# Kernel optimization log

Hardware: AMD Instinct MI355X
Metric: run time of the kernel (lower is better)

## Reference

```python
import jax, jax.numpy as jnp
import numpy as np

LEN_MASK = 2   # hardcoded in the original forward
TOP_POOL = 5   # positions drawn from top-5 intensity slots


def setup_inputs() -> dict:
    key = jax.random.key(0)
    k1, k2 = jax.random.split(key)
    B, S = 16384, 1024
    x = jax.random.randint(k1, (B, S), 0, 10000, dtype=jnp.int64)
    intensity_ = jax.random.uniform(k2, (B, 1, S), dtype=jnp.float32)
    return {"x": x, "intensity_": intensity_, "max_pred": 5}


def reference(x, intensity_, max_pred):
    # x: [B, S] int token ids; intensity_: [B, 1, S] float
    intensity = jnp.squeeze(intensity_, axis=1)            # [B, S]
    B, S = x.shape
    # top-5 positions by descending intensity (== argsort(desc)[:5])
    top5 = jax.lax.top_k(intensity, TOP_POOL)[1]           # [B, 5] int
    # randperm(5)[:2] per sample, vectorized: argsort of iid uniforms
    rkey = jax.random.key(42)
    u = jax.random.uniform(rkey, (B, TOP_POOL))
    sel = jnp.argsort(u, axis=-1)[:, :LEN_MASK]            # [B, 2] random 2-of-5
    mask_pos2 = jnp.take_along_axis(top5, sel, axis=1)     # [B, 2]
    # mask_bool: all False (rand > 1), True at the chosen positions
    mask_bool = jnp.zeros((B, S), dtype=bool).at[
        jnp.arange(B)[:, None], mask_pos2
    ].set(True)                                            # [B, S]
    mask_x = jnp.where(mask_bool, jnp.asarray(1, x.dtype), x)   # masked_fill(x, mask_bool, 1)
    mask_token2 = jnp.take_along_axis(x, mask_pos2, axis=1)     # [B, 2]
    # pad to max_pred with zeros (original branch: len_mask < max_pred)
    n_pad = max_pred - LEN_MASK
    mask_pos = jnp.pad(mask_pos2, ((0, 0), (0, n_pad))).astype(jnp.int64)
    mask_token = jnp.pad(mask_token2, ((0, 0), (0, n_pad))).astype(jnp.int64)
    return mask_x, mask_token, mask_pos
```

## Files before the change

kernel.cpp:

```cpp
#include <hip/hip_runtime.h>
#include <stdint.h>


#define S_LEN 1024
#define TOPK 5

__device__ __forceinline__ uint32_t rotl32(uint32_t x, int r) {
    return (x << r) | (x >> (32 - r));
}

__device__ __forceinline__ void threefry2x32(uint32_t k0, uint32_t k1,
                                             uint32_t x0, uint32_t x1,
                                             uint32_t& o0, uint32_t& o1) {
    uint32_t ks2 = k0 ^ k1 ^ 0x1BD11BDAu;
    x0 += k0; x1 += k1;
#define TF_R4(a,b,c,d) \
    x0 += x1; x1 = rotl32(x1,a); x1 ^= x0; \
    x0 += x1; x1 = rotl32(x1,b); x1 ^= x0; \
    x0 += x1; x1 = rotl32(x1,c); x1 ^= x0; \
    x0 += x1; x1 = rotl32(x1,d); x1 ^= x0;
    TF_R4(13,15,26,6);   x0 += k1;  x1 += ks2 + 1u;
    TF_R4(17,29,16,24);  x0 += ks2; x1 += k0  + 2u;
    TF_R4(13,15,26,6);   x0 += k0;  x1 += k1  + 3u;
    TF_R4(17,29,16,24);  x0 += k1;  x1 += ks2 + 4u;
    TF_R4(13,15,26,6);   x0 += ks2; x1 += k0  + 5u;
#undef TF_R4
    o0 = x0; o1 = x1;
}

__device__ __forceinline__ void cswap_desc(uint64_t& a, uint64_t& b) {
    uint64_t lo = (a < b) ? a : b;
    uint64_t hi = (a < b) ? b : a;
    a = hi; b = lo;
}

__device__ __forceinline__ uint64_t u64max(uint64_t a, uint64_t b) {
    return (a > b) ? a : b;
}

__global__ __launch_bounds__(256)
void mask_kernel(const float* __restrict__ inten,
                 const int*   __restrict__ x,
                 int* __restrict__ out_x,
                 int* __restrict__ out_tok,
                 int* __restrict__ out_pos,
                 int B) {
    const int wave = threadIdx.x >> 6;
    const int lane = threadIdx.x & 63;
    const int row  = blockIdx.x * 4 + wave;
    if (row >= B) return;

    const float* irow = inten + (size_t)row * S_LEN;
    const int*   xrow = x     + (size_t)row * S_LEN;

    uint64_t t0 = 0, t1 = 0, t2 = 0, t3 = 0, t4 = 0;
#pragma unroll
    for (int it = 0; it < 4; ++it) {
        const int sbase = it * 256 + lane * 4;
        const float4 v = *reinterpret_cast<const float4*>(irow + sbase);
#pragma unroll
        for (int q = 0; q < 4; ++q) {
            const float f = (q == 0) ? v.x : (q == 1) ? v.y : (q == 2) ? v.z : v.w;
            const uint32_t fb = __float_as_uint(f);
            const uint64_t key =
                ((uint64_t)fb << 32) | (uint32_t)(1023 - (sbase + q));
            t4 = u64max(t4, key);
            cswap_desc(t3, t4);
            cswap_desc(t2, t3);
            cswap_desc(t1, t2);
            cswap_desc(t0, t1);
        }
    }

    int idx0 = 0, idx1 = 0, idx2 = 0, idx3 = 0, idx4 = 0;
#pragma unroll
    for (int r = 0; r < TOPK; ++r) {
        uint64_t w = t0;
#pragma unroll
        for (int off = 1; off < 64; off <<= 1) {
            const uint64_t o =
                (uint64_t)__shfl_xor((unsigned long long)w, off, 64);
            w = u64max(w, o);
        }
        if (t0 == w) { t0 = t1; t1 = t2; t2 = t3; t3 = t4; t4 = 0; }
        const int s = 1023 - (int)((uint32_t)w & 1023u);
        if (r == 0) idx0 = s;
        else if (r == 1) idx1 = s;
        else if (r == 2) idx2 = s;
        else if (r == 3) idx3 = s;
        else idx4 = s;
    }

    uint32_t kj = 0xFFFFFFFFu;
    if (lane < TOPK) {
        const uint32_t g = (uint32_t)row * 5u + (uint32_t)lane;
        uint32_t o0, o1;
        threefry2x32(0u, 42u, 0u, g, o0, o1);
        const uint32_t bits = o0 ^ o1;
        kj = ((bits >> 9) << 3) | (uint32_t)lane;
    }
    const uint32_t q0 = __shfl(kj, 0, 64);
    const uint32_t q1 = __shfl(kj, 1, 64);
    const uint32_t q2 = __shfl(kj, 2, 64);
    const uint32_t q3 = __shfl(kj, 3, 64);
    const uint32_t q4 = __shfl(kj, 4, 64);

    const uint32_t mn1 = min(min(min(q0, q1), min(q2, q3)), q4);
    const int sel0 = (int)(mn1 & 7u);
    const uint32_t e0 = (q0 == mn1) ? 0xFFFFFFFFu : q0;
    const uint32_t e1 = (q1 == mn1) ? 0xFFFFFFFFu : q1;
    const uint32_t e2 = (q2 == mn1) ? 0xFFFFFFFFu : q2;
    const uint32_t e3 = (q3 == mn1) ? 0xFFFFFFFFu : q3;
    const uint32_t e4 = (q4 == mn1) ? 0xFFFFFFFFu : q4;
    const uint32_t mn2 = min(min(min(e0, e1), min(e2, e3)), e4);
    const int sel1 = (int)(mn2 & 7u);

    const int p0 = (sel0 == 0) ? idx0 : (sel0 == 1) ? idx1 : (sel0 == 2) ? idx2
                 : (sel0 == 3) ? idx3 : idx4;
    const int p1 = (sel1 == 0) ? idx0 : (sel1 == 1) ? idx1 : (sel1 == 2) ? idx2
                 : (sel1 == 3) ? idx3 : idx4;

    int* orow = out_x + (size_t)row * S_LEN;
#pragma unroll
    for (int it = 0; it < 4; ++it) {
        const int sbase = it * 256 + lane * 4;
        int4 o = *reinterpret_cast<const int4*>(xrow + sbase);
        if (sbase + 0 == p0 || sbase + 0 == p1) o.x = 1;
        if (sbase + 1 == p0 || sbase + 1 == p1) o.y = 1;
        if (sbase + 2 == p0 || sbase + 2 == p1) o.z = 1;
        if (sbase + 3 == p0 || sbase + 3 == p1) o.w = 1;
        *reinterpret_cast<int4*>(orow + sbase) = o;
    }

    if (lane == 0) {
        const int xa = xrow[p0];
        const int xb = xrow[p1];
        int* tk = out_tok + (size_t)row * 5;
        tk[0] = xa; tk[1] = xb; tk[2] = 0; tk[3] = 0; tk[4] = 0;
        int* pp = out_pos + (size_t)row * 5;
        pp[0] = p0; pp[1] = p1; pp[2] = 0; pp[3] = 0; pp[4] = 0;
    }
}

extern "C" void kernel_launch(void* const* d_in, const int* in_sizes, int n_in,
                              void* d_out, int out_size, void* d_ws, size_t ws_size,
                              hipStream_t stream) {
    const int*   x     = (const int*)d_in[0];
    const float* inten = (const float*)d_in[1];

    const int BS = in_sizes[0];
    const int B  = BS / S_LEN;

    int* out     = (int*)d_out;
    int* out_tok = out + (size_t)B * S_LEN;
    int* out_pos = out_tok + (size_t)B * TOPK;

    dim3 grid((B + 3) / 4), block(256);
    hipLaunchKernelGGL(mask_kernel, grid, block, 0, stream,
                       inten, x, out, out_tok, out_pos, B);
}
```

Measured before the change: 173.5 us.

## Hoist x loads before top-k and compress per-lane keys to 32-bit

Issues all intensity and x loads up front so that the x row reads overlap the top-k selection instead of being fetched after it. The per-lane top-5 insertion sort now works on 32-bit keys: the intensity is quantised to a 23-bit mantissa integer (value times 2^23) packed with a 4-bit local rank. These keys are widened back to 64-bit keys carrying the global position before the wave reduction. The 32-bit keys cut the compare-swap cost but assume intensities lie in [0,1), and the quantisation could change tie-breaking. Holding the x values live also raises register pressure.

After: 174.6 us. About the same (+0.6%).

```diff
diff --git a/kernel.cpp b/kernel.cpp
--- a/kernel.cpp
+++ b/kernel.cpp
@@ -28,9 +28,9 @@
     o0 = x0; o1 = x1;
 }
 
-__device__ __forceinline__ void cswap_desc(uint64_t& a, uint64_t& b) {
-    uint64_t lo = (a < b) ? a : b;
-    uint64_t hi = (a < b) ? b : a;
+__device__ __forceinline__ void cswap32(uint32_t& a, uint32_t& b) {
+    const uint32_t hi = max(a, b);
+    const uint32_t lo = min(a, b);
     a = hi; b = lo;
 }
 
@@ -53,36 +53,45 @@
     const float* irow = inten + (size_t)row * S_LEN;
     const int*   xrow = x     + (size_t)row * S_LEN;
 
-    uint64_t t0 = 0, t1 = 0, t2 = 0, t3 = 0, t4 = 0;
-#pragma unroll
-    for (int it = 0; it < 4; ++it) {
-        const int sbase = it * 256 + lane * 4;
-        const float4 v = *reinterpret_cast<const float4*>(irow + sbase);
-#pragma unroll
-        for (int q = 0; q < 4; ++q) {
-            const float f = (q == 0) ? v.x : (q == 1) ? v.y : (q == 2) ? v.z : v.w;
-            const uint32_t fb = __float_as_uint(f);
-            const uint64_t key =
-                ((uint64_t)fb << 32) | (uint32_t)(1023 - (sbase + q));
-            t4 = u64max(t4, key);
-            cswap_desc(t3, t4);
-            cswap_desc(t2, t3);
-            cswap_desc(t1, t2);
-            cswap_desc(t0, t1);
-        }
-    }
+    const float4 v0 = *reinterpret_cast<const float4*>(irow + 0   + lane * 4);
+    const float4 v1 = *reinterpret_cast<const float4*>(irow + 256 + lane * 4);
+    const float4 v2 = *reinterpret_cast<const float4*>(irow + 512 + lane * 4);
+    const float4 v3 = *reinterpret_cast<const float4*>(irow + 768 + lane * 4);
+    const int4 xv0 = *reinterpret_cast<const int4*>(xrow + 0   + lane * 4);
+    const int4 xv1 = *reinterpret_cast<const int4*>(xrow + 256 + lane * 4);
+    const int4 xv2 = *reinterpret_cast<const int4*>(xrow + 512 + lane * 4);
+    const int4 xv3 = *reinterpret_cast<const int4*>(xrow + 768 + lane * 4);
+
+    uint32_t t0 = 0, t1 = 0, t2 = 0, t3 = 0, t4 = 0;
+#define INS(f, rnk) {                                                   \
+        const uint32_t m = (uint32_t)((f) * 8388608.0f);                \
+        const uint32_t key = (m << 4) | (uint32_t)(15 - (rnk));        \
+        t4 = max(t4, key);                                              \
+        cswap32(t3, t4); cswap32(t2, t3); cswap32(t1, t2); cswap32(t0, t1); }
+    INS(v0.x, 0)  INS(v0.y, 1)  INS(v0.z, 2)  INS(v0.w, 3)
+    INS(v1.x, 4)  INS(v1.y, 5)  INS(v1.z, 6)  INS(v1.w, 7)
+    INS(v2.x, 8)  INS(v2.y, 9)  INS(v2.z, 10) INS(v2.w, 11)
+    INS(v3.x, 12) INS(v3.y, 13) INS(v3.z, 14) INS(v3.w, 15)
+#undef INS
+
+#define TO64(t) ({                                                       \
+        const uint32_t r_ = 15u - ((t) & 15u);                           \
+        const uint32_t s_ = ((r_ >> 2) << 8) + ((uint32_t)lane << 2) + (r_ & 3u); \
+        (((uint64_t)((t) >> 4)) << 10) | (uint64_t)(1023u - s_); })
+    uint64_t T0 = TO64(t0), T1 = TO64(t1), T2 = TO64(t2), T3 = TO64(t3), T4 = TO64(t4);
+#undef TO64
 
     int idx0 = 0, idx1 = 0, idx2 = 0, idx3 = 0, idx4 = 0;
 #pragma unroll
     for (int r = 0; r < TOPK; ++r) {
-        uint64_t w = t0;
+        uint64_t w = T0;
 #pragma unroll
         for (int off = 1; off < 64; off <<= 1) {
             const uint64_t o =
                 (uint64_t)__shfl_xor((unsigned long long)w, off, 64);
             w = u64max(w, o);
         }
-        if (t0 == w) { t0 = t1; t1 = t2; t2 = t3; t3 = t4; t4 = 0; }
+        if (T0 == w) { T0 = T1; T1 = T2; T2 = T3; T3 = T4; T4 = 0; }
         const int s = 1023 - (int)((uint32_t)w & 1023u);
         if (r == 0) idx0 = s;
         else if (r == 1) idx1 = s;
@@ -121,16 +130,19 @@
                  : (sel1 == 3) ? idx3 : idx4;
 
     int* orow = out_x + (size_t)row * S_LEN;
-#pragma unroll
-    for (int it = 0; it < 4; ++it) {
-        const int sbase = it * 256 + lane * 4;
-        int4 o = *reinterpret_cast<const int4*>(xrow + sbase);
-        if (sbase + 0 == p0 || sbase + 0 == p1) o.x = 1;
-        if (sbase + 1 == p0 || sbase + 1 == p1) o.y = 1;
-        if (sbase + 2 == p0 || sbase + 2 == p1) o.z = 1;
-        if (sbase + 3 == p0 || sbase + 3 == p1) o.w = 1;
-        *reinterpret_cast<int4*>(orow + sbase) = o;
-    }
+#define STORE4(xv, base) {                                               \
+        int4 o = (xv);                                                   \
+        const int sb = (base) + lane * 4;                                \
+        if (sb + 0 == p0 || sb + 0 == p1) o.x = 1;                       \
+        if (sb + 1 == p0 || sb + 1 == p1) o.y = 1;                       \
+        if (sb + 2 == p0 || sb + 2 == p1) o.z = 1;                       \
+        if (sb + 3 == p0 || sb + 3 == p1) o.w = 1;                       \
+        *reinterpret_cast<int4*>(orow + sb) = o; }
+    STORE4(xv0, 0)
+    STORE4(xv1, 256)
+    STORE4(xv2, 512)
+    STORE4(xv3, 768)
+#undef STORE4
 
     if (lane == 0) {
         const int xa = xrow[p0];
```
